# Kernel tuning notes

Measured on AMD Instinct MI355X. Metric: run time of the kernel, lower is better.

Reference implementation:

```python
import jax, jax.numpy as jnp
import numpy as np

B, S, H = 2, 2048, 1024
NH, NKV, HD = 16, 4, 64
G, R = NKV, NH // NKV  # 4 kv groups, 4 query heads per group


def setup_inputs() -> dict:
    key = jax.random.key(0)
    ks = jax.random.split(key, 7)
    scale = 1.0 / np.sqrt(H)
    return {
        "hidden_states": jax.random.normal(ks[0], (B, S, H), jnp.float32),
        "cos": jax.random.normal(ks[1], (S, HD), jnp.float32),
        "sin": jax.random.normal(ks[2], (S, HD), jnp.float32),
        "attention_mask": jnp.ones((B, S), jnp.float32),
        "Wq": jax.random.normal(ks[3], (H, NH * HD), jnp.float32) * scale,
        "Wk": jax.random.normal(ks[4], (H, NKV * HD), jnp.float32) * scale,
        "Wv": jax.random.normal(ks[5], (H, NKV * HD), jnp.float32) * scale,
        "Wo": jax.random.normal(ks[6], (NH * HD, H), jnp.float32) * scale,
    }


def _rotate_half(x):
    h = x.shape[-1] // 2
    return jnp.concatenate([-x[..., h:], x[..., :h]], axis=-1)


def reference(hidden_states, cos, sin, attention_mask, Wq, Wk, Wv, Wo):
    x = hidden_states
    q = (x @ Wq).reshape(B, S, NH, HD)
    k = (x @ Wk).reshape(B, S, NKV, HD)
    v = (x @ Wv).reshape(B, S, NKV, HD)
    # RoPE: cos/sin [S,HD] broadcast over batch and heads
    c = cos[None, :, None, :]
    s = sin[None, :, None, :]
    q = q * c + _rotate_half(q) * s
    k = k * c + _rotate_half(k) * s
    # GQA without materializing repeated KV: q grouped as [B,S,G,R,HD]
    qg = q.reshape(B, S, G, R, HD)
    scores = jnp.einsum("bsgrd,btgd->bgrst", qg, k) / np.sqrt(HD)  # [B,G,R,S,T]
    causal = jnp.tril(jnp.ones((S, S), bool))
    scores = jnp.where(causal[None, None, None], scores, -jnp.inf)
    scores = scores + ((1.0 - attention_mask) * -1e9)[:, None, None, None, :]
    probs = jax.nn.softmax(scores.astype(jnp.float32), axis=-1).astype(q.dtype)
    out = jnp.einsum("bgrst,btgd->bsgrd", probs, v).reshape(B, S, NH * HD)
    return out @ Wo
```

## Files before the change

### kernel.cpp

```cpp
#include <hip/hip_runtime.h>
#include <math.h>

#define B_   2
#define S_   2048
#define H_   1024
#define NH_  16
#define NKV_ 4
#define HD_  64
#define R_   (NH_ / NKV_)
#define QKVW 1536

typedef __attribute__((ext_vector_type(8))) short bf16x8;
typedef __attribute__((ext_vector_type(4))) float f32x4;

__device__ inline short f2bf(float f) {
    unsigned u = __float_as_uint(f);
    u += 0x7FFF + ((u >> 16) & 1);
    return (short)(u >> 16);
}

__device__ inline void gload_lds16(const void* gptr, void* lptr) {
    __builtin_amdgcn_global_load_lds(
        (const __attribute__((address_space(1))) unsigned int*)gptr,
        (__attribute__((address_space(3))) unsigned int*)lptr,
        16, 0, 0);
}

__global__ __launch_bounds__(256) void tconv_all(const float* __restrict__ Wq,
                                                 const float* __restrict__ Wk,
                                                 const float* __restrict__ Wv,
                                                 const float* __restrict__ Wo,
                                                 short* __restrict__ Wqkvt,
                                                 short* __restrict__ Wot) {
    __shared__ short T[64][68];
    const int bx = blockIdx.x;
    const float* W; short* Wt; int N, idx;
    if (bx < 256)      { W = Wq; Wt = Wqkvt;                     N = 1024; idx = bx; }
    else if (bx < 320) { W = Wk; Wt = Wqkvt + 1024 * 1024;       N = 256;  idx = bx - 256; }
    else if (bx < 384) { W = Wv; Wt = Wqkvt + 1280 * 1024;       N = 256;  idx = bx - 320; }
    else               { W = Wo; Wt = Wot;                       N = 1024; idx = bx - 384; }
    const int ntiles = N >> 6;
    const int n0 = (idx % ntiles) * 64;
    const int k0 = (idx / ntiles) * 64;

    const int tid = threadIdx.x;
    const int r  = tid >> 4;
    const int c4 = (tid & 15) * 4;
#pragma unroll
    for (int t = 0; t < 4; t++) {
        int row = t * 16 + r;
        float4 v = *(const float4*)&W[(size_t)(k0 + row) * N + n0 + c4];
        T[c4 + 0][row] = f2bf(v.x);
        T[c4 + 1][row] = f2bf(v.y);
        T[c4 + 2][row] = f2bf(v.z);
        T[c4 + 3][row] = f2bf(v.w);
    }
    __syncthreads();
#pragma unroll
    for (int t = 0; t < 4; t++) {
        int row = t * 16 + r;
        short4 o = *(short4*)&T[row][c4];
        *(short4*)&Wt[(size_t)(n0 + row) * 1024 + k0 + c4] = o;
    }
}

__global__ __launch_bounds__(256) void gemm1_fused(const float* __restrict__ x,
                                                   const short* __restrict__ Bt,
                                                   short* __restrict__ qkv,
                                                   short* __restrict__ Vtg,
                                                   const float* __restrict__ cosb,
                                                   const float* __restrict__ sinb) {
    __shared__ short Ah[64 * 32];
    __shared__ short Bh[128 * 32];

    const int tid  = threadIdx.x;
    const int w    = tid >> 6;
    const int lane = tid & 63;
    const int ln   = lane & 15;
    const int qd   = lane >> 4;
    const int wr   = w >> 1, wc = w & 1;
    const int row0 = blockIdx.y * 64;
    const int col0 = blockIdx.x * 128;

    const int sr = lane >> 2;
    const int sk = (lane & 3) * 8;
    const int ar  = tid >> 2;
    const int ac8 = (tid & 3) * 8;

    f32x4 acc[2][4];
#pragma unroll
    for (int mi = 0; mi < 2; mi++)
#pragma unroll
        for (int ni = 0; ni < 4; ni++)
            acc[mi][ni] = (f32x4){0.f, 0.f, 0.f, 0.f};

    for (int k0 = 0; k0 < 1024; k0 += 32) {
        __syncthreads();
        {
            const float* xp = x + (size_t)(row0 + ar) * H_ + k0 + ac8;
            float4 a = *(const float4*)xp;
            float4 b2 = *(const float4*)(xp + 4);
            bf16x8 o;
            o[0] = f2bf(a.x);  o[1] = f2bf(a.y);  o[2] = f2bf(a.z);  o[3] = f2bf(a.w);
            o[4] = f2bf(b2.x); o[5] = f2bf(b2.y); o[6] = f2bf(b2.z); o[7] = f2bf(b2.w);
            *(bf16x8*)&Ah[ar * 32 + ac8] = o;
        }
        gload_lds16(Bt + (size_t)(col0 + w * 32 + sr) * 1024 + k0 + sk, &Bh[(w * 32) * 32]);
        gload_lds16(Bt + (size_t)(col0 + w * 32 + 16 + sr) * 1024 + k0 + sk, &Bh[(w * 32 + 16) * 32]);
        __syncthreads();

        bf16x8 af[2], bfr[4];
#pragma unroll
        for (int mi = 0; mi < 2; mi++)
            af[mi] = *(const bf16x8*)&Ah[(wr * 32 + mi * 16 + ln) * 32 + qd * 8];
#pragma unroll
        for (int ni = 0; ni < 4; ni++)
            bfr[ni] = *(const bf16x8*)&Bh[(wc * 64 + ni * 16 + ln) * 32 + qd * 8];
#pragma unroll
        for (int mi = 0; mi < 2; mi++)
#pragma unroll
            for (int ni = 0; ni < 4; ni++)
                acc[mi][ni] = __builtin_amdgcn_mfma_f32_16x16x32_bf16(af[mi], bfr[ni], acc[mi][ni], 0, 0, 0);
    }

    const int colw = col0 + wc * 64;
    if (colw < H_ + NKV_ * HD_) {
#pragma unroll
        for (int mi = 0; mi < 2; mi++)
#pragma unroll
            for (int i = 0; i < 4; i++) {
                const int row  = row0 + wr * 32 + mi * 16 + qd * 4 + i;
                const int spos = row & (S_ - 1);
                const float* cp = cosb + (size_t)spos * HD_;
                const float* sp = sinb + (size_t)spos * HD_;
                float o0[4];
#pragma unroll
                for (int ni = 0; ni < 2; ni++) {
                    const int d = ni * 16 + ln;
                    float x0 = acc[mi][ni][i], x1 = acc[mi][ni + 2][i];
                    o0[ni]     = x0 * cp[d]      - x1 * sp[d];
                    o0[ni + 2] = x1 * cp[d + 32] + x0 * sp[d + 32];
                }
                short* Cp = qkv + (size_t)row * QKVW + colw + ln;
#pragma unroll
                for (int ni = 0; ni < 4; ni++) Cp[ni * 16] = f2bf(o0[ni]);
            }
    } else {
        const int g = (colw - (H_ + NKV_ * HD_)) >> 6;
#pragma unroll
        for (int mi = 0; mi < 2; mi++) {
            const int rbase = row0 + wr * 32 + mi * 16 + qd * 4;
            const int bg = ((rbase >> 11) * NKV_) + g;
            const int s0 = rbase & (S_ - 1);
#pragma unroll
            for (int ni = 0; ni < 4; ni++) {
                const int d = ni * 16 + ln;
                short4 pk = { f2bf(acc[mi][ni][0]), f2bf(acc[mi][ni][1]),
                              f2bf(acc[mi][ni][2]), f2bf(acc[mi][ni][3]) };
                *(short4*)&Vtg[((size_t)bg * HD_ + d) * S_ + s0] = pk;
            }
        }
    }
}

__global__ __launch_bounds__(256) void gemm2_bt(const short* __restrict__ A, int lda,
                                                const short* __restrict__ Bt,
                                                float* __restrict__ C, int ldc,
                                                int K) {
    __shared__ short Ah[64 * 32];
    __shared__ short Bh[128 * 32];

    const int tid  = threadIdx.x;
    const int w    = tid >> 6;
    const int lane = tid & 63;
    const int ln   = lane & 15;
    const int qd   = lane >> 4;
    const int wr   = w >> 1, wc = w & 1;
    const int row0 = blockIdx.y * 64;
    const int col0 = blockIdx.x * 128;

    const int sr = lane >> 2;
    const int sk = (lane & 3) * 8;

    f32x4 acc[2][4];
#pragma unroll
    for (int mi = 0; mi < 2; mi++)
#pragma unroll
        for (int ni = 0; ni < 4; ni++)
            acc[mi][ni] = (f32x4){0.f, 0.f, 0.f, 0.f};

    for (int k0 = 0; k0 < K; k0 += 32) {
        __syncthreads();
        gload_lds16(A + (size_t)(row0 + w * 16 + sr) * lda + k0 + sk, &Ah[(w * 16) * 32]);
        gload_lds16(Bt + (size_t)(col0 + w * 32 + sr) * K + k0 + sk, &Bh[(w * 32) * 32]);
        gload_lds16(Bt + (size_t)(col0 + w * 32 + 16 + sr) * K + k0 + sk, &Bh[(w * 32 + 16) * 32]);
        __syncthreads();

        bf16x8 af[2], bfr[4];
#pragma unroll
        for (int mi = 0; mi < 2; mi++)
            af[mi] = *(const bf16x8*)&Ah[(wr * 32 + mi * 16 + ln) * 32 + qd * 8];
#pragma unroll
        for (int ni = 0; ni < 4; ni++)
            bfr[ni] = *(const bf16x8*)&Bh[(wc * 64 + ni * 16 + ln) * 32 + qd * 8];
#pragma unroll
        for (int mi = 0; mi < 2; mi++)
#pragma unroll
            for (int ni = 0; ni < 4; ni++)
                acc[mi][ni] = __builtin_amdgcn_mfma_f32_16x16x32_bf16(af[mi], bfr[ni], acc[mi][ni], 0, 0, 0);
    }

#pragma unroll
    for (int mi = 0; mi < 2; mi++)
#pragma unroll
        for (int i = 0; i < 4; i++) {
            const size_t row = row0 + wr * 32 + mi * 16 + qd * 4 + i;
            float* Cp = C + row * ldc + col0 + wc * 64 + ln;
#pragma unroll
            for (int ni = 0; ni < 4; ni++) Cp[ni * 16] = acc[mi][ni][i];
        }
}

__global__ __launch_bounds__(512, 2) void attn_kernel(short* __restrict__ qkv,
                                                      const short* __restrict__ Vtg,
                                                      const float* __restrict__ maskb) {
    const int tid  = threadIdx.x;
    const int w    = tid >> 6;
    const int lane = tid & 63;
    const int ln   = lane & 15;
    const int qd   = lane >> 4;

    const int fid = blockIdx.x;
    const int bg  = fid & 7;
    const int u   = fid >> 3;
    const int b   = bg >> 2;
    const int g   = bg & 3;
    const int h   = g * R_ + (u & 3);
    const int a   = u >> 2;

    const int qt   = (w < 4) ? a : (15 - a);
    const int st   = w & 3;
    const int rowb = qt * 128 + st * 32;
    const int ktd  = 2 * qt + (st >> 1);
    const int nt   = 32 - 2 * a;

    __shared__ short Ks[2][64 * 72];
    __shared__ short Vt[2][64 * 72];
    __shared__ short Ps[8][16 * 72];
    __shared__ float mskS[2][64];
    short* const ps = Ps[w];

    const short* const Kb = qkv + (size_t)b * S_ * QKVW + H_ + g * HD_;
    const short* const Vb = Vtg + (size_t)bg * HD_ * S_;
    const float* const mb = maskb + b * S_;

    const int fr = tid >> 3;
    const int fc = (tid & 7) * 8;

    bf16x8 qf[2][2];
#pragma unroll
    for (int rg = 0; rg < 2; rg++) {
        const short* qp = qkv + (size_t)(b * S_ + rowb + rg * 16 + ln) * QKVW + h * HD_;
        qf[rg][0] = *(const bf16x8*)&qp[qd * 8];
        qf[rg][1] = *(const bf16x8*)&qp[32 + qd * 8];
    }

    f32x4 O[2][4] = {};
    float mrow[2] = {-1e30f, -1e30f};
    float lrow[2] = {0.0f, 0.0f};

    *(bf16x8*)&Ks[0][fr * 72 + fc] = *(const bf16x8*)&Kb[(size_t)fr * QKVW + fc];
    *(bf16x8*)&Vt[0][fr * 72 + fc] = *(const bf16x8*)&Vb[(size_t)fr * S_ + fc];
    if (tid < 64) mskS[0][tid] = mb[tid];
    __syncthreads();

    int cur = 0;
    for (int kt = 0; kt < nt; kt++) {
        const int base = kt * 64;
        const bool pf = (kt + 1 < nt);

        bf16x8 pk, pv;
        float pm = 0.0f;
        if (pf) {
            const int nb = base + 64;
            pk = *(const bf16x8*)&Kb[(size_t)(nb + fr) * QKVW + fc];
            pv = *(const bf16x8*)&Vb[(size_t)fr * S_ + nb + fc];
            if (tid < 64) pm = mb[nb + tid];
        }

        if (kt <= ktd) {
            f32x4 St[2][4];
#pragma unroll
            for (int kg = 0; kg < 4; kg++) {
                bf16x8 ka0 = *(const bf16x8*)&Ks[cur][(kg * 16 + ln) * 72 + qd * 8];
                bf16x8 ka1 = *(const bf16x8*)&Ks[cur][(kg * 16 + ln) * 72 + 32 + qd * 8];
#pragma unroll
                for (int rg = 0; rg < 2; rg++) {
                    f32x4 z = {0.f, 0.f, 0.f, 0.f};
                    z = __builtin_amdgcn_mfma_f32_16x16x32_bf16(ka0, qf[rg][0], z, 0, 0, 0);
                    St[rg][kg] = __builtin_amdgcn_mfma_f32_16x16x32_bf16(ka1, qf[rg][1], z, 0, 0, 0);
                }
            }

            bf16x8 vb[2][4];
#pragma unroll
            for (int kc2 = 0; kc2 < 2; kc2++)
#pragma unroll
                for (int dt = 0; dt < 4; dt++)
                    vb[kc2][dt] = *(const bf16x8*)&Vt[cur][(dt * 16 + ln) * 72 + kc2 * 32 + qd * 8];

            float mt[4][4];
#pragma unroll
            for (int kg = 0; kg < 4; kg++) {
                float4 mv = *(const float4*)&mskS[cur][kg * 16 + qd * 4];
                mt[kg][0] = (1.0f - mv.x) * -1e9f;
                mt[kg][1] = (1.0f - mv.y) * -1e9f;
                mt[kg][2] = (1.0f - mv.z) * -1e9f;
                mt[kg][3] = (1.0f - mv.w) * -1e9f;
            }

            const bool diag = (kt == ktd);

#pragma unroll
            for (int rg = 0; rg < 2; rg++) {
                const int qrow = rowb + rg * 16 + ln;
                float sc[4][4];
#pragma unroll
                for (int kg = 0; kg < 4; kg++) {
                    const int keyb = base + kg * 16 + qd * 4;
#pragma unroll
                    for (int i = 0; i < 4; i++) {
                        float v = fmaf(St[rg][kg][i], 0.125f, mt[kg][i]);
                        sc[kg][i] = (diag && (keyb + i > qrow)) ? -1e30f : v;
                    }
                }
                float mx = sc[0][0];
#pragma unroll
                for (int kg = 0; kg < 4; kg++)
#pragma unroll
                    for (int i = 0; i < 4; i++) mx = fmaxf(mx, sc[kg][i]);
                mx = fmaxf(mx, __shfl_xor(mx, 16));
                mx = fmaxf(mx, __shfl_xor(mx, 32));

                if (__ballot(mx > mrow[rg] + 8.0f)) {
                    float nm    = fmaxf(mrow[rg], mx);
                    float alpha = __expf(mrow[rg] - nm);
                    lrow[rg] *= alpha;
#pragma unroll
                    for (int i = 0; i < 4; i++) {
                        float av = __shfl(alpha, qd * 4 + i);
#pragma unroll
                        for (int dt = 0; dt < 4; dt++) O[rg][dt][i] *= av;
                    }
                    mrow[rg] = nm;
                }
                const float nm = mrow[rg];

                float ls = 0.0f;
#pragma unroll
                for (int kg = 0; kg < 4; kg++)
#pragma unroll
                    for (int i = 0; i < 4; i++) {
                        float p = __expf(sc[kg][i] - nm);
                        sc[kg][i] = p;
                        ls += p;
                    }
                ls += __shfl_xor(ls, 16);
                ls += __shfl_xor(ls, 32);
                lrow[rg] += ls;

#pragma unroll
                for (int kg = 0; kg < 4; kg++) {
                    short4 pk2 = { f2bf(sc[kg][0]), f2bf(sc[kg][1]),
                                   f2bf(sc[kg][2]), f2bf(sc[kg][3]) };
                    *(short4*)&ps[ln * 72 + kg * 16 + qd * 4] = pk2;
                }

#pragma unroll
                for (int kc2 = 0; kc2 < 2; kc2++) {
                    bf16x8 pa = *(const bf16x8*)&ps[ln * 72 + kc2 * 32 + qd * 8];
#pragma unroll
                    for (int dt = 0; dt < 4; dt++)
                        O[rg][dt] = __builtin_amdgcn_mfma_f32_16x16x32_bf16(pa, vb[kc2][dt], O[rg][dt], 0, 0, 0);
                }
            }
        }

        if (pf) {
            const int nxt = cur ^ 1;
            *(bf16x8*)&Ks[nxt][fr * 72 + fc] = pk;
            *(bf16x8*)&Vt[nxt][fr * 72 + fc] = pv;
            if (tid < 64) mskS[nxt][tid] = pm;
        }
        __syncthreads();
        cur ^= 1;
    }

#pragma unroll
    for (int rg = 0; rg < 2; rg++)
#pragma unroll
        for (int i = 0; i < 4; i++) {
            float li  = __shfl(lrow[rg], qd * 4 + i);
            float inv = 1.0f / li;
            const int row = rowb + rg * 16 + qd * 4 + i;
            short* op = qkv + (size_t)(b * S_ + row) * QKVW + h * HD_ + ln;
#pragma unroll
            for (int dt = 0; dt < 4; dt++) op[dt * 16] = f2bf(O[rg][dt][i] * inv);
        }
}

extern "C" void kernel_launch(void* const* d_in, const int* in_sizes, int n_in,
                              void* d_out, int out_size, void* d_ws, size_t ws_size,
                              hipStream_t stream) {
    const float* x     = (const float*)d_in[0];
    const float* cosb  = (const float*)d_in[1];
    const float* sinb  = (const float*)d_in[2];
    const float* maskb = (const float*)d_in[3];
    const float* Wq    = (const float*)d_in[4];
    const float* Wk    = (const float*)d_in[5];
    const float* Wv    = (const float*)d_in[6];
    const float* Wo    = (const float*)d_in[7];

    const int M = B_ * S_;

    short* qkv   = (short*)d_ws;
    short* Wqkvt = qkv + (size_t)M * QKVW;
    short* Wot   = Wqkvt + (size_t)QKVW * H_;
    short* Vtg   = Wot + (size_t)H_ * H_;
    float* out   = (float*)d_out;

    dim3 blk(256);

    tconv_all<<<dim3(640), blk, 0, stream>>>(Wq, Wk, Wv, Wo, Wqkvt, Wot);

    gemm1_fused<<<dim3(QKVW / 128, M / 64), blk, 0, stream>>>(x, Wqkvt, qkv, Vtg, cosb, sinb);

    attn_kernel<<<dim3(256), dim3(512), 0, stream>>>(qkv, Vtg, maskb);

    gemm2_bt<<<dim3(H_ / 128, M / 64), blk, 0, stream>>>(qkv, QKVW, Wot, out, H_, H_);
}
```

Baseline: 201.0 us.

## Pre-convert activations to bf16 and enlarge GEMM tiles to 128x128

Adds blocks to the weight-conversion kernel that convert the fp32 hidden states to bf16 into the output buffer, used as scratch. The QKV GEMM can then load A tiles with direct global-to-LDS loads instead of converting in its main loop. Both projection GEMMs grow from 64x128 to 128x128 tiles with a 4x4 MFMA accumulator per wave, which halves the grid and raises data reuse per block. The cost is higher register pressure, fewer blocks for occupancy, and an extra pass over x.

```diff
diff --git a/kernel.cpp b/kernel.cpp
--- a/kernel.cpp
+++ b/kernel.cpp
@@ -31,9 +31,28 @@
                                                  const float* __restrict__ Wv,
                                                  const float* __restrict__ Wo,
                                                  short* __restrict__ Wqkvt,
-                                                 short* __restrict__ Wot) {
+                                                 short* __restrict__ Wot,
+                                                 const float* __restrict__ x,
+                                                 short* __restrict__ xb) {
+    const int bx = blockIdx.x;
+    const int tid = threadIdx.x;
+
+    if (bx >= 640) {
+        const size_t e0 = (size_t)(bx - 640) * 16384;
+#pragma unroll
+        for (int t = 0; t < 8; t++) {
+            const size_t i = e0 + ((size_t)t * 256 + tid) * 8;
+            float4 a = *(const float4*)&x[i];
+            float4 c = *(const float4*)&x[i + 4];
+            bf16x8 o;
+            o[0] = f2bf(a.x); o[1] = f2bf(a.y); o[2] = f2bf(a.z); o[3] = f2bf(a.w);
+            o[4] = f2bf(c.x); o[5] = f2bf(c.y); o[6] = f2bf(c.z); o[7] = f2bf(c.w);
+            *(bf16x8*)&xb[i] = o;
+        }
+        return;
+    }
+
     __shared__ short T[64][68];
-    const int bx = blockIdx.x;
     const float* W; short* Wt; int N, idx;
     if (bx < 256)      { W = Wq; Wt = Wqkvt;                     N = 1024; idx = bx; }
     else if (bx < 320) { W = Wk; Wt = Wqkvt + 1024 * 1024;       N = 256;  idx = bx - 256; }
@@ -43,7 +62,6 @@
     const int n0 = (idx % ntiles) * 64;
     const int k0 = (idx / ntiles) * 64;
 
-    const int tid = threadIdx.x;
     const int r  = tid >> 4;
     const int c4 = (tid & 15) * 4;
 #pragma unroll
@@ -64,13 +82,13 @@
     }
 }
 
-__global__ __launch_bounds__(256) void gemm1_fused(const float* __restrict__ x,
+__global__ __launch_bounds__(256) void gemm1_fused(const short* __restrict__ xb,
                                                    const short* __restrict__ Bt,
                                                    short* __restrict__ qkv,
                                                    short* __restrict__ Vtg,
                                                    const float* __restrict__ cosb,
                                                    const float* __restrict__ sinb) {
-    __shared__ short Ah[64 * 32];
+    __shared__ short Ah[128 * 32];
     __shared__ short Bh[128 * 32];
 
     const int tid  = threadIdx.x;
@@ -79,57 +97,48 @@
     const int ln   = lane & 15;
     const int qd   = lane >> 4;
     const int wr   = w >> 1, wc = w & 1;
-    const int row0 = blockIdx.y * 64;
+    const int row0 = blockIdx.y * 128;
     const int col0 = blockIdx.x * 128;
 
     const int sr = lane >> 2;
     const int sk = (lane & 3) * 8;
-    const int ar  = tid >> 2;
-    const int ac8 = (tid & 3) * 8;
-
-    f32x4 acc[2][4];
-#pragma unroll
-    for (int mi = 0; mi < 2; mi++)
+
+    f32x4 acc[4][4];
+#pragma unroll
+    for (int mi = 0; mi < 4; mi++)
 #pragma unroll
         for (int ni = 0; ni < 4; ni++)
             acc[mi][ni] = (f32x4){0.f, 0.f, 0.f, 0.f};
 
     for (int k0 = 0; k0 < 1024; k0 += 32) {
         __syncthreads();
-        {
-            const float* xp = x + (size_t)(row0 + ar) * H_ + k0 + ac8;
-            float4 a = *(const float4*)xp;
-            float4 b2 = *(const float4*)(xp + 4);
-            bf16x8 o;
-            o[0] = f2bf(a.x);  o[1] = f2bf(a.y);  o[2] = f2bf(a.z);  o[3] = f2bf(a.w);
-            o[4] = f2bf(b2.x); o[5] = f2bf(b2.y); o[6] = f2bf(b2.z); o[7] = f2bf(b2.w);
-            *(bf16x8*)&Ah[ar * 32 + ac8] = o;
-        }
-        gload_lds16(Bt + (size_t)(col0 + w * 32 + sr) * 1024 + k0 + sk, &Bh[(w * 32) * 32]);
-        gload_lds16(Bt + (size_t)(col0 + w * 32 + 16 + sr) * 1024 + k0 + sk, &Bh[(w * 32 + 16) * 32]);
+        gload_lds16(xb + (size_t)(row0 + w * 16 + sr) * 1024 + k0 + sk,      &Ah[(w * 16) * 32]);
+        gload_lds16(xb + (size_t)(row0 + 64 + w * 16 + sr) * 1024 + k0 + sk, &Ah[(64 + w * 16) * 32]);
+        gload_lds16(Bt + (size_t)(col0 + w * 16 + sr) * 1024 + k0 + sk,      &Bh[(w * 16) * 32]);
+        gload_lds16(Bt + (size_t)(col0 + 64 + w * 16 + sr) * 1024 + k0 + sk, &Bh[(64 + w * 16) * 32]);
         __syncthreads();
 
-        bf16x8 af[2], bfr[4];
-#pragma unroll
-        for (int mi = 0; mi < 2; mi++)
-            af[mi] = *(const bf16x8*)&Ah[(wr * 32 + mi * 16 + ln) * 32 + qd * 8];
+        bf16x8 af[4], bf[4];
+#pragma unroll
+        for (int mi = 0; mi < 4; mi++)
+            af[mi] = *(const bf16x8*)&Ah[(wr * 64 + mi * 16 + ln) * 32 + qd * 8];
 #pragma unroll
         for (int ni = 0; ni < 4; ni++)
-            bfr[ni] = *(const bf16x8*)&Bh[(wc * 64 + ni * 16 + ln) * 32 + qd * 8];
-#pragma unroll
-        for (int mi = 0; mi < 2; mi++)
+            bf[ni] = *(const bf16x8*)&Bh[(wc * 64 + ni * 16 + ln) * 32 + qd * 8];
+#pragma unroll
+        for (int mi = 0; mi < 4; mi++)
 #pragma unroll
             for (int ni = 0; ni < 4; ni++)
-                acc[mi][ni] = __builtin_amdgcn_mfma_f32_16x16x32_bf16(af[mi], bfr[ni], acc[mi][ni], 0, 0, 0);
+                acc[mi][ni] = __builtin_amdgcn_mfma_f32_16x16x32_bf16(af[mi], bf[ni], acc[mi][ni], 0, 0, 0);
     }
 
     const int colw = col0 + wc * 64;
     if (colw < H_ + NKV_ * HD_) {
 #pragma unroll
-        for (int mi = 0; mi < 2; mi++)
+        for (int mi = 0; mi < 4; mi++)
 #pragma unroll
             for (int i = 0; i < 4; i++) {
-                const int row  = row0 + wr * 32 + mi * 16 + qd * 4 + i;
+                const int row  = row0 + wr * 64 + mi * 16 + qd * 4 + i;
                 const int spos = row & (S_ - 1);
                 const float* cp = cosb + (size_t)spos * HD_;
                 const float* sp = sinb + (size_t)spos * HD_;
@@ -148,8 +157,8 @@
     } else {
         const int g = (colw - (H_ + NKV_ * HD_)) >> 6;
 #pragma unroll
-        for (int mi = 0; mi < 2; mi++) {
-            const int rbase = row0 + wr * 32 + mi * 16 + qd * 4;
+        for (int mi = 0; mi < 4; mi++) {
+            const int rbase = row0 + wr * 64 + mi * 16 + qd * 4;
             const int bg = ((rbase >> 11) * NKV_) + g;
             const int s0 = rbase & (S_ - 1);
 #pragma unroll
@@ -167,7 +176,7 @@
                                                 const short* __restrict__ Bt,
                                                 float* __restrict__ C, int ldc,
                                                 int K) {
-    __shared__ short Ah[64 * 32];
+    __shared__ short Ah[128 * 32];
     __shared__ short Bh[128 * 32];
 
     const int tid  = threadIdx.x;
@@ -176,45 +185,46 @@
     const int ln   = lane & 15;
     const int qd   = lane >> 4;
     const int wr   = w >> 1, wc = w & 1;
-    const int row0 = blockIdx.y * 64;
+    const int row0 = blockIdx.y * 128;
     const int col0 = blockIdx.x * 128;
 
     const int sr = lane >> 2;
     const int sk = (lane & 3) * 8;
 
-    f32x4 acc[2][4];
-#pragma unroll
-    for (int mi = 0; mi < 2; mi++)
+    f32x4 acc[4][4];
+#pragma unroll
+    for (int mi = 0; mi < 4; mi++)
 #pragma unroll
         for (int ni = 0; ni < 4; ni++)
             acc[mi][ni] = (f32x4){0.f, 0.f, 0.f, 0.f};
 
     for (int k0 = 0; k0 < K; k0 += 32) {
         __syncthreads();
-        gload_lds16(A + (size_t)(row0 + w * 16 + sr) * lda + k0 + sk, &Ah[(w * 16) * 32]);
-        gload_lds16(Bt + (size_t)(col0 + w * 32 + sr) * K + k0 + sk, &Bh[(w * 32) * 32]);
-        gload_lds16(Bt + (size_t)(col0 + w * 32 + 16 + sr) * K + k0 + sk, &Bh[(w * 32 + 16) * 32]);
+        gload_lds16(A + (size_t)(row0 + w * 16 + sr) * lda + k0 + sk,      &Ah[(w * 16) * 32]);
+        gload_lds16(A + (size_t)(row0 + 64 + w * 16 + sr) * lda + k0 + sk, &Ah[(64 + w * 16) * 32]);
+        gload_lds16(Bt + (size_t)(col0 + w * 16 + sr) * K + k0 + sk,       &Bh[(w * 16) * 32]);
+        gload_lds16(Bt + (size_t)(col0 + 64 + w * 16 + sr) * K + k0 + sk,  &Bh[(64 + w * 16) * 32]);
         __syncthreads();
 
-        bf16x8 af[2], bfr[4];
-#pragma unroll
-        for (int mi = 0; mi < 2; mi++)
-            af[mi] = *(const bf16x8*)&Ah[(wr * 32 + mi * 16 + ln) * 32 + qd * 8];
+        bf16x8 af[4], bf[4];
+#pragma unroll
+        for (int mi = 0; mi < 4; mi++)
+            af[mi] = *(const bf16x8*)&Ah[(wr * 64 + mi * 16 + ln) * 32 + qd * 8];
 #pragma unroll
         for (int ni = 0; ni < 4; ni++)
-            bfr[ni] = *(const bf16x8*)&Bh[(wc * 64 + ni * 16 + ln) * 32 + qd * 8];
-#pragma unroll
-        for (int mi = 0; mi < 2; mi++)
+            bf[ni] = *(const bf16x8*)&Bh[(wc * 64 + ni * 16 + ln) * 32 + qd * 8];
+#pragma unroll
+        for (int mi = 0; mi < 4; mi++)
 #pragma unroll
             for (int ni = 0; ni < 4; ni++)
-                acc[mi][ni] = __builtin_amdgcn_mfma_f32_16x16x32_bf16(af[mi], bfr[ni], acc[mi][ni], 0, 0, 0);
-    }
-
-#pragma unroll
-    for (int mi = 0; mi < 2; mi++)
+                acc[mi][ni] = __builtin_amdgcn_mfma_f32_16x16x32_bf16(af[mi], bf[ni], acc[mi][ni], 0, 0, 0);
+    }
+
+#pragma unroll
+    for (int mi = 0; mi < 4; mi++)
 #pragma unroll
         for (int i = 0; i < 4; i++) {
-            const size_t row = row0 + wr * 32 + mi * 16 + qd * 4 + i;
+            const size_t row = row0 + wr * 64 + mi * 16 + qd * 4 + i;
             float* Cp = C + row * ldc + col0 + wc * 64 + ln;
 #pragma unroll
             for (int ni = 0; ni < 4; ni++) Cp[ni * 16] = acc[mi][ni][i];
@@ -427,15 +437,16 @@
     short* Wqkvt = qkv + (size_t)M * QKVW;
     short* Wot   = Wqkvt + (size_t)QKVW * H_;
     short* Vtg   = Wot + (size_t)H_ * H_;
+    short* xb    = (short*)d_out;
     float* out   = (float*)d_out;
 
     dim3 blk(256);
 
-    tconv_all<<<dim3(640), blk, 0, stream>>>(Wq, Wk, Wv, Wo, Wqkvt, Wot);
-
-    gemm1_fused<<<dim3(QKVW / 128, M / 64), blk, 0, stream>>>(x, Wqkvt, qkv, Vtg, cosb, sinb);
+    tconv_all<<<dim3(896), blk, 0, stream>>>(Wq, Wk, Wv, Wo, Wqkvt, Wot, x, xb);
+
+    gemm1_fused<<<dim3(QKVW / 128, M / 128), blk, 0, stream>>>(xb, Wqkvt, qkv, Vtg, cosb, sinb);
 
     attn_kernel<<<dim3(256), dim3(512), 0, stream>>>(qkv, Vtg, maskb);
 
-    gemm2_bt<<<dim3(H_ / 128, M / 64), blk, 0, stream>>>(qkv, QKVW, Wot, out, H_, H_);
-}
+    gemm2_bt<<<dim3(H_ / 128, M / 128), blk, 0, stream>>>(qkv, QKVW, Wot, out, H_, H_);
+}
```

Result: slower. 206.6 us (+2.8%).
